# Optimization experiments

Measured on AMD Instinct MI355X. Metric: run time of the kernel, lower is better.

Reference implementation:

```python
import jax, jax.numpy as jnp
import numpy as np

OMEGA_ENC = 0.01   # Encoder.omega
OMEGA_K = 0.1      # KernelMLP.omega
N0, E0 = 4096, 16384     # level-0 graph
N1, E1 = 1024, 8192      # level-1 (pooled) graph
F_IN, H, LAT, DIM = 8, 64, 32, 3
F = H + DIM              # conv input features (x || pos)


def _glorot(key, shape):
    s = jnp.sqrt(2.0 / (shape[0] + shape[-1]))
    return (jax.random.normal(key, shape) * s).astype(jnp.float32)


def setup_inputs() -> dict:
    key = jax.random.key(0)
    ks = jax.random.split(key, 24)
    inp = {
        "x": jax.random.normal(ks[0], (N0, F_IN), jnp.float32),
        "pos": jax.random.normal(ks[1], (N0, DIM), jnp.float32),
        "edge_index": jax.random.randint(ks[2], (2, E0), 0, N0),
        "pool_edge_index1": jax.random.randint(ks[3], (2, E1), 0, N1),
        "pool_pos1": jax.random.normal(ks[4], (N1, DIM), jnp.float32),
        "pool_keep_idx0": jnp.sort(jax.random.randint(ks[5], (N1,), 0, N0)),
        "lin0_w": _glorot(ks[6], (F_IN, H)),
        "lin0_b": 0.01 * jax.random.normal(ks[7], (H,), jnp.float32),
        "lin1_w": _glorot(ks[8], (H, LAT)),
        "lin1_b": 0.01 * jax.random.normal(ks[9], (LAT,), jnp.float32),
    }
    k = 10
    for i in range(2):
        inp[f"conv{i}_k_w0"] = _glorot(ks[k], (DIM + 1, H))
        inp[f"conv{i}_k_b0"] = 0.01 * jax.random.normal(ks[k + 1], (H,), jnp.float32)
        inp[f"conv{i}_k_w1"] = _glorot(ks[k + 2], (H, H))
        inp[f"conv{i}_k_b1"] = 0.01 * jax.random.normal(ks[k + 3], (H,), jnp.float32)
        inp[f"conv{i}_k_w2"] = _glorot(ks[k + 4], (H, F))
        inp[f"conv{i}_k_b2"] = 0.01 * jax.random.normal(ks[k + 5], (F,), jnp.float32)
        inp[f"conv{i}_bias"] = jnp.zeros((H,), jnp.float32)  # zeros() init in torch
        k += 6
    return inp


def _with_self_loops(ei, n):
    # add_remaining_self_loops: input edges are assumed self-loop-free
    loops = jnp.arange(n, dtype=ei.dtype)
    return jnp.concatenate([ei, jnp.stack([loops, loops])], axis=1)


def _kernel_conv(xf, ei, pos, n, w0, b0, w1, b1, w2, b2, bias):
    src, dst = ei[0], ei[1]
    rel = pos[dst] - pos[src]                               # [E,3]
    zero = jnp.all(rel == 0.0, axis=1)                      # self loops -> rho=0, nan phi in torch
    rel_s = jnp.where(zero[:, None], 1.0, rel)              # safe values (avoid nan grads)
    rho = jnp.sqrt(jnp.sum(rel_s * rel_s, axis=1))
    theta = jnp.arctan2(rel_s[:, 1], rel_s[:, 0])
    phi = jnp.arcsin(jnp.clip(rel_s[:, 2] / rho, -1.0, 1.0))
    # torch sets theta/phi to 0 where phi is nan (rho==0); rho itself is 0 there
    rho = jnp.where(zero, 0.0, rho)
    theta = jnp.where(zero, 0.0, theta)
    phi = jnp.where(zero, 0.0, phi)
    feats = jnp.stack([rho, theta / jnp.pi, phi / jnp.pi], axis=1)   # [E,3]
    # KernelMLP lin0 on (feats || channel_id), evaluated for all out channels at once
    base = feats @ w0[:DIM] + b0                            # [E,H]
    ch = jnp.arange(H, dtype=xf.dtype)                      # out_channels == H
    h0 = jnp.sin(OMEGA_K * (base[None] + ch[:, None, None] * w0[DIM][None, None]))  # [C,E,H]
    h1 = jnp.sin(OMEGA_K * (jnp.einsum('ceh,hk->cek', h0, w1) + b1))                # [C,E,H]
    x_j = xf[src]                                           # [E,F]
    # msg[e,c] = (lin2(h1[c,e]) * x_j[e]).sum(); lin2 folded into the contraction
    msg = jnp.einsum('ceh,hf,ef->ec', h1, w2, x_j) + (x_j @ b2)[:, None]            # [E,C]
    return jax.ops.segment_sum(msg, dst, num_segments=n) + bias


def reference(x, edge_index, pos, pool_edge_index1, pool_pos1, pool_keep_idx0,
              lin0_w, lin0_b, lin1_w, lin1_b,
              conv0_k_w0, conv0_k_b0, conv0_k_w1, conv0_k_b1, conv0_k_w2, conv0_k_b2, conv0_bias,
              conv1_k_w0, conv1_k_b0, conv1_k_w1, conv1_k_b1, conv1_k_w2, conv1_k_b2, conv1_bias):
    n0 = x.shape[0]
    h = jnp.sin(OMEGA_ENC * (x @ lin0_w + lin0_b))
    ei0 = _with_self_loops(edge_index, n0)
    h = jnp.sin(OMEGA_ENC * _kernel_conv(jnp.concatenate([h, pos], 1), ei0, pos, n0,
                                         conv0_k_w0, conv0_k_b0, conv0_k_w1, conv0_k_b1,
                                         conv0_k_w2, conv0_k_b2, conv0_bias))
    # max_pool_neighbor_x: per-node max over neighbors incl. self (self loops in ei0)
    h = jax.ops.segment_max(h[ei0[0]], ei0[1], num_segments=n0)[pool_keep_idx0]
    n1 = pool_pos1.shape[0]
    ei1 = _with_self_loops(pool_edge_index1, n1)
    h = jnp.sin(OMEGA_ENC * _kernel_conv(jnp.concatenate([h, pool_pos1], 1), ei1, pool_pos1, n1,
                                         conv1_k_w0, conv1_k_b0, conv1_k_w1, conv1_k_b1,
                                         conv1_k_w2, conv1_k_b2, conv1_bias))
    return jnp.sin(OMEGA_ENC * (h @ lin1_w + lin1_b))   # [N1, LAT]
```

## Files before the change

kernel.cpp:

```cpp
#include <hip/hip_runtime.h>
#include <hip/hip_fp16.h>

#define N0C 4096
#define E0C 16384
#define N1C 1024
#define E1C 8192
#define HC 64
#define FINC 8
#define LATC 32
#define FC 67
#define E0T (E0C + N0C)
#define E1T (E1C + N1C)

typedef float f32x4 __attribute__((ext_vector_type(4)));
typedef _Float16 f16x8 __attribute__((ext_vector_type(8)));

__global__ __launch_bounds__(256) void k_prep(
    const float* __restrict__ x, const float* __restrict__ l0w,
    const float* __restrict__ l0b, const float* __restrict__ posp,
    const float* __restrict__ c0w2, const float* __restrict__ c0b2,
    const float* __restrict__ c0w0, const float* __restrict__ c1w0,
    const float* __restrict__ c0w1, const float* __restrict__ c1w1,
    const int* __restrict__ ei0, const int* __restrict__ ei1,
    _Float16* __restrict__ bC0, _Float16* __restrict__ bS0,
    _Float16* __restrict__ bC1, _Float16* __restrict__ bS1,
    _Float16* __restrict__ w1f0, _Float16* __restrict__ w1f1,
    int* __restrict__ cnt, float* __restrict__ tN, float* __restrict__ dN) {
  if (blockIdx.x < 1024) {
    __shared__ float w2s[64][69];
    __shared__ float xr[4][64];
    const int tid = threadIdx.x;
    const int wave = __builtin_amdgcn_readfirstlane(tid >> 6), lane = tid & 63;
    for (int idx = tid; idx < HC * FC; idx += 256)
      w2s[idx / FC][idx % FC] = c0w2[idx];
    const int n = blockIdx.x * 4 + wave;
    float a = l0b[lane];
#pragma unroll
    for (int f = 0; f < FINC; ++f) a = fmaf(x[n * FINC + f], l0w[f * HC + lane], a);
    xr[wave][lane] = sinf(0.01f * a);
    __syncthreads();
    const float px = posp[n * 3], py = posp[n * 3 + 1], pz = posp[n * 3 + 2];
    float tl = 0.f, ds = 0.f;
#pragma unroll 8
    for (int f = 0; f < HC; ++f) {
      float xv = xr[wave][f];
      tl = fmaf(xv, w2s[lane][f], tl);
      ds = fmaf(xv, c0b2[f], ds);
    }
    tl = fmaf(px, w2s[lane][64], fmaf(py, w2s[lane][65], fmaf(pz, w2s[lane][66], tl)));
    ds = fmaf(px, c0b2[64], fmaf(py, c0b2[65], fmaf(pz, c0b2[66], ds)));
    tN[n * HC + lane] = tl;
    if (lane == 0) dN[n] = ds;
  } else {
    int id = (blockIdx.x - 1024) * 256 + threadIdx.x;
    if (id < 8192) {
      int lvl = id >> 12, r = id & 4095;
      int fi = r >> 9, lane = (r >> 3) & 63, j = r & 7;
      int nt = fi & 3, ks = fi >> 2;
      int c = nt * 16 + (lane & 15);
      int h = ks * 32 + (lane >> 4) * 8 + j;
      const float* w = lvl ? c1w0 : c0w0;
      float s, cv;
      sincosf(0.1f * (float)c * w[3 * HC + h], &s, &cv);
      (lvl ? bC1 : bC0)[r] = (_Float16)cv;
      (lvl ? bS1 : bS0)[r] = (_Float16)s;
    } else if (id < 16384) {
      int r0 = id - 8192;
      int lvl = r0 >> 12, r = r0 & 4095;
      int fi = r >> 9, lane = (r >> 3) & 63, j = r & 7;
      int ms = fi & 3, ks = fi >> 2;
      int h = ks * 32 + (lane >> 4) * 8 + j;
      int kout = ms * 16 + (lane & 15);
      const float* w = lvl ? c1w1 : c0w1;
      (lvl ? w1f1 : w1f0)[r] = (_Float16)(0.1f * w[h * HC + kout]);
    } else if (id < 16384 + E0T + E1T) {
      int r = id - 16384;
      if (r < E0T) {
        int dst = (r < E0C) ? ei0[E0C + r] : (r - E0C);
        atomicAdd(cnt + dst, 1);
      } else {
        int e = r - E0T;
        int dst = (e < E1C) ? ei1[E1C + e] : (e - E1C);
        atomicAdd(cnt + N0C + dst, 1);
      }
    }
  }
}

__global__ void k_scan(const int* __restrict__ cnt, int* __restrict__ rp0,
                       int* __restrict__ rp1) {
  __shared__ int wsum[16];
  const int b = blockIdx.x;
  const int n = b ? N1C : N0C;
  const int* c = cnt + (b ? N0C : 0);
  int* rp = b ? rp1 : rp0;
  const int tid = threadIdx.x;
  const int lane = tid & 63, wid = tid >> 6;
  const int per = n >> 10;
  int loc[4];
  int sum = 0;
  for (int j = 0; j < per; ++j) { loc[j] = c[tid * per + j]; sum += loc[j]; }
  int xv = sum;
#pragma unroll
  for (int off = 1; off < 64; off <<= 1) {
    int v = __shfl_up(xv, off, 64);
    if (lane >= off) xv += v;
  }
  if (lane == 63) wsum[wid] = xv;
  __syncthreads();
  if (wid == 0) {
    int w = (lane < 16) ? wsum[lane] : 0;
#pragma unroll
    for (int off = 1; off < 16; off <<= 1) {
      int v = __shfl_up(w, off, 64);
      if (lane >= off) w += v;
    }
    if (lane < 16) wsum[lane] = w;
  }
  __syncthreads();
  int prefix = wid ? wsum[wid - 1] : 0;
  int incl = xv + prefix;
  int base = incl - sum;
  for (int j = 0; j < per; ++j) { rp[tid * per + j] = base; base += loc[j]; }
  if (tid == 1023) rp[n] = incl;
}

__global__ void k_scatter(const int* __restrict__ ei0, const int* __restrict__ ei1,
                          const int* __restrict__ rp0, const int* __restrict__ rp1,
                          int* __restrict__ fill, int* __restrict__ eidx0,
                          int* __restrict__ eidx1) {
  int id = blockIdx.x * blockDim.x + threadIdx.x;
  if (id < E0T) {
    int dst = (id < E0C) ? ei0[E0C + id] : (id - E0C);
    eidx0[rp0[dst] + atomicAdd(fill + dst, 1)] = id;
  } else if (id < E0T + E1T) {
    int e = id - E0T;
    int dst = (e < E1C) ? ei1[E1C + e] : (e - E1C);
    eidx1[rp1[dst] + atomicAdd(fill + N0C + dst, 1)] = e;
  }
}

__global__ __launch_bounds__(256, 3) void k_conv(
    const int* __restrict__ ei, int E,
    const float* __restrict__ posp,
    const float* __restrict__ tN, const float* __restrict__ dN,
    const float* __restrict__ kw0, const float* __restrict__ kb0,
    const _Float16* __restrict__ bC, const _Float16* __restrict__ bS,
    const _Float16* __restrict__ w1f, const float* __restrict__ b1,
    float* __restrict__ msg) {
  __shared__ __attribute__((aligned(16))) _Float16 bCs[4096], bSs[4096];
  __shared__ __attribute__((aligned(16))) _Float16 scS[4][2][64], scC[4][2][64];
  const int tid = threadIdx.x;
  const int wave = __builtin_amdgcn_readfirstlane(tid >> 6), lane = tid & 63;
  const int q = lane >> 4;
  for (int idx = tid; idx < 512; idx += 256) {
    ((f16x8*)bCs)[idx] = ((const f16x8*)bC)[idx];
    ((f16x8*)bSs)[idx] = ((const f16x8*)bS)[idx];
  }
  f16x8 w1r[8];
#pragma unroll
  for (int f = 0; f < 8; ++f) w1r[f] = *(const f16x8*)(w1f + ((f << 6) + lane) * 8);
  f32x4 bbq[4];
#pragma unroll
  for (int ms = 0; ms < 4; ++ms) {
    f32x4 t = *(const f32x4*)(b1 + ms * 16 + q * 4);
    bbq[ms] = t * 0.1f;
  }
  const float kb0v = kb0[lane];
  const float kw0x = kw0[lane], kw0y = kw0[HC + lane], kw0z = kw0[2 * HC + lane];
  __syncthreads();

  const int e0 = (blockIdx.x * 4 + wave) * 4;

  auto stg = [&](int e, int& sN, float& sv, float& cv, float& dv) {
    int s, d2;
    if (e < E) { s = ei[e]; d2 = ei[E + e]; } else { s = e - E; d2 = s; }
    sN = s;
    const float px = posp[s * 3], py = posp[s * 3 + 1], pz = posp[s * 3 + 2];
    const float rx = posp[d2 * 3] - px;
    const float ry = posp[d2 * 3 + 1] - py;
    const float rz = posp[d2 * 3 + 2] - pz;
    float f0 = 0.f, f1 = 0.f, f2 = 0.f;
    if (!(rx == 0.f && ry == 0.f && rz == 0.f)) {
      const float PI_F = 3.14159265358979323846f;
      float rho = sqrtf(rx * rx + ry * ry + rz * rz);
      float th = atan2f(ry, rx);
      float ratio = fminf(1.f, fmaxf(-1.f, rz / rho));
      float ph = asinf(ratio);
      f0 = rho; f1 = th / PI_F; f2 = ph / PI_F;
    }
    float base = fmaf(f0, kw0x, fmaf(f1, kw0y, fmaf(f2, kw0z, kb0v)));
    sincosf(0.1f * base, &sv, &cv);
    dv = dN[s];
  };

  int s0;
  float sv0, cv0, dv0;
  stg(e0, s0, sv0, cv0, dv0);
#pragma unroll
  for (int i = 0; i < 4; ++i) {
    const int buf = i & 1;
    scS[wave][buf][lane] = (_Float16)sv0;
    scC[wave][buf][lane] = (_Float16)cv0;
    __builtin_amdgcn_wave_barrier();
    f32x4 tr[4];
    {
      const float* trp = tN + (size_t)s0 * HC;
#pragma unroll
      for (int ms = 0; ms < 4; ++ms) tr[ms] = *(const f32x4*)(trp + ms * 16 + q * 4);
    }
    int s1 = 0;
    float sv1 = 0.f, cv1 = 0.f, dv1 = 0.f;
    if (i < 3) stg(e0 + i + 1, s1, sv1, cv1, dv1);

    f32x4 acc[4][4];
#pragma unroll
    for (int ms = 0; ms < 4; ++ms)
#pragma unroll
      for (int nt = 0; nt < 4; ++nt) acc[ms][nt] = bbq[ms];
#pragma unroll
    for (int ks = 0; ks < 2; ++ks) {
      f16x8 sv8 = *(const f16x8*)&scS[wave][buf][ks * 32 + q * 8];
      f16x8 cv8 = *(const f16x8*)&scC[wave][buf][ks * 32 + q * 8];
      f16x8 bf[4];
#pragma unroll
      for (int nt = 0; nt < 4; ++nt) {
        f16x8 cb = *(const f16x8*)&bCs[((ks * 4 + nt) * 64 + lane) * 8];
        f16x8 sb = *(const f16x8*)&bSs[((ks * 4 + nt) * 64 + lane) * 8];
        bf[nt] = sv8 * cb + cv8 * sb;
      }
#pragma unroll
      for (int ms = 0; ms < 4; ++ms)
#pragma unroll
        for (int nt = 0; nt < 4; ++nt)
          acc[ms][nt] = __builtin_amdgcn_mfma_f32_16x16x32_f16(
              w1r[ks * 4 + ms], bf[nt], acc[ms][nt], 0, 0, 0);
    }

    float snt0 = 0.f, snt1 = 0.f, snt2 = 0.f, snt3 = 0.f;
#pragma unroll
    for (int ms = 0; ms < 4; ++ms) {
#pragma unroll
      for (int r = 0; r < 4; ++r) {
        float tt = tr[ms][r];
        snt0 = fmaf(__sinf(acc[ms][0][r]), tt, snt0);
        snt1 = fmaf(__sinf(acc[ms][1][r]), tt, snt1);
        snt2 = fmaf(__sinf(acc[ms][2][r]), tt, snt2);
        snt3 = fmaf(__sinf(acc[ms][3][r]), tt, snt3);
      }
    }
    snt0 += __shfl_xor(snt0, 16, 64); snt0 += __shfl_xor(snt0, 32, 64);
    snt1 += __shfl_xor(snt1, 16, 64); snt1 += __shfl_xor(snt1, 32, 64);
    snt2 += __shfl_xor(snt2, 16, 64); snt2 += __shfl_xor(snt2, 32, 64);
    snt3 += __shfl_xor(snt3, 16, 64); snt3 += __shfl_xor(snt3, 32, 64);
    float val = (q == 0) ? snt0 : (q == 1) ? snt1 : (q == 2) ? snt2 : snt3;
    msg[(size_t)(e0 + i) * HC + lane] = val + dv0;
    s0 = s1; sv0 = sv1; cv0 = cv1; dv0 = dv1;
  }
}

__global__ void k_reduce0(const float* __restrict__ msg, const int* __restrict__ eidx,
                          const int* __restrict__ rp, const float* __restrict__ bias,
                          float* __restrict__ hc) {
  const int wave = threadIdx.x >> 6, lane = threadIdx.x & 63;
  const int n = blockIdx.x * 4 + wave;
  const int j0 = rp[n], j1 = rp[n + 1];
  float a0 = 0.f, a1 = 0.f;
  int j = j0;
  for (; j + 1 < j1; j += 2) {
    int ea = eidx[j], eb = eidx[j + 1];
    a0 += msg[(size_t)ea * HC + lane];
    a1 += msg[(size_t)eb * HC + lane];
  }
  if (j < j1) a0 += msg[(size_t)eidx[j] * HC + lane];
  hc[(size_t)n * HC + lane] = sinf(0.01f * (a0 + a1 + bias[lane]));
}

__global__ void k_pool1(const float* __restrict__ hc0, const int* __restrict__ eidx,
                        const int* __restrict__ rp, const int* __restrict__ ei,
                        const int* __restrict__ keep, const float* __restrict__ ppos,
                        const float* __restrict__ c1w2, const float* __restrict__ c1b2,
                        float* __restrict__ tN, float* __restrict__ dN) {
  __shared__ float w2s[64][69];
  __shared__ float xr[4][64];
  const int tid = threadIdx.x;
  const int wave = __builtin_amdgcn_readfirstlane(tid >> 6), lane = tid & 63;
  for (int idx = tid; idx < HC * FC; idx += 256)
    w2s[idx / FC][idx % FC] = c1w2[idx];
  const int i = blockIdx.x * 4 + wave;
  int n = keep[i];
  int j0 = rp[n], j1 = rp[n + 1];
  float m = -INFINITY;
  for (int j = j0; j < j1; ++j) {
    int e = eidx[j];
    int src = (e < E0C) ? ei[e] : (e - E0C);
    m = fmaxf(m, hc0[(size_t)src * HC + lane]);
  }
  xr[wave][lane] = m;
  __syncthreads();
  const float px = ppos[i * 3], py = ppos[i * 3 + 1], pz = ppos[i * 3 + 2];
  float tl = 0.f, ds = 0.f;
#pragma unroll 8
  for (int f = 0; f < HC; ++f) {
    float xv = xr[wave][f];
    tl = fmaf(xv, w2s[lane][f], tl);
    ds = fmaf(xv, c1b2[f], ds);
  }
  tl = fmaf(px, w2s[lane][64], fmaf(py, w2s[lane][65], fmaf(pz, w2s[lane][66], tl)));
  ds = fmaf(px, c1b2[64], fmaf(py, c1b2[65], fmaf(pz, c1b2[66], ds)));
  tN[i * HC + lane] = tl;
  if (lane == 0) dN[i] = ds;
}

__global__ void k_reduce1f(const float* __restrict__ msg, const int* __restrict__ eidx,
                           const int* __restrict__ rp, const float* __restrict__ bias,
                           const float* __restrict__ l1w, const float* __restrict__ l1b,
                           float* __restrict__ outp) {
  __shared__ float hr[4][64];
  const int wave = threadIdx.x >> 6, lane = threadIdx.x & 63;
  const int node = blockIdx.x * 4 + wave;
  const int j0 = rp[node], j1 = rp[node + 1];
  float a0 = 0.f, a1 = 0.f;
  int j = j0;
  for (; j + 1 < j1; j += 2) {
    int ea = eidx[j], eb = eidx[j + 1];
    a0 += msg[(size_t)ea * HC + lane];
    a1 += msg[(size_t)eb * HC + lane];
  }
  if (j < j1) a0 += msg[(size_t)eidx[j] * HC + lane];
  hr[wave][lane] = sinf(0.01f * (a0 + a1 + bias[lane]));
  __syncthreads();
  if (lane < LATC) {
    const float* h = hr[wave];
    float o = l1b[lane];
#pragma unroll 8
    for (int c = 0; c < HC; ++c) o = fmaf(h[c], l1w[c * LATC + lane], o);
    outp[node * LATC + lane] = sinf(0.01f * o);
  }
}

extern "C" void kernel_launch(void* const* d_in, const int* in_sizes, int n_in,
                              void* d_out, int out_size, void* d_ws, size_t ws_size,
                              hipStream_t stream) {
  (void)in_sizes; (void)n_in; (void)out_size; (void)ws_size;
  const float* x    = (const float*)d_in[0];
  const float* pos  = (const float*)d_in[1];
  const int*   ei   = (const int*)d_in[2];
  const int*   pei  = (const int*)d_in[3];
  const float* ppos = (const float*)d_in[4];
  const int*   keep = (const int*)d_in[5];
  const float* l0w  = (const float*)d_in[6];
  const float* l0b  = (const float*)d_in[7];
  const float* l1w  = (const float*)d_in[8];
  const float* l1b  = (const float*)d_in[9];
  const float* c0w0 = (const float*)d_in[10];
  const float* c0b0 = (const float*)d_in[11];
  const float* c0w1 = (const float*)d_in[12];
  const float* c0b1 = (const float*)d_in[13];
  const float* c0w2 = (const float*)d_in[14];
  const float* c0b2 = (const float*)d_in[15];
  const float* c0bias = (const float*)d_in[16];
  const float* c1w0 = (const float*)d_in[17];
  const float* c1b0 = (const float*)d_in[18];
  const float* c1w1 = (const float*)d_in[19];
  const float* c1b1 = (const float*)d_in[20];
  const float* c1w2 = (const float*)d_in[21];
  const float* c1b2 = (const float*)d_in[22];
  const float* c1bias = (const float*)d_in[23];
  float* outp = (float*)d_out;

  char* p = (char*)d_ws;
  auto carve = [&](size_t bytes) -> char* {
    char* r = p;
    p += (bytes + 255) & ~(size_t)255;
    return r;
  };
  float* hc0  = (float*)carve((size_t)N0C * HC * 4);
  float* tN0  = (float*)carve((size_t)N0C * HC * 4);
  float* dN0  = (float*)carve((size_t)N0C * 4);
  float* tN1  = (float*)carve((size_t)N1C * HC * 4);
  float* dN1  = (float*)carve((size_t)N1C * 4);
  _Float16* bC0  = (_Float16*)carve(4096 * 2);
  _Float16* bS0  = (_Float16*)carve(4096 * 2);
  _Float16* bC1  = (_Float16*)carve(4096 * 2);
  _Float16* bS1  = (_Float16*)carve(4096 * 2);
  _Float16* w1f0 = (_Float16*)carve(4096 * 2);
  _Float16* w1f1 = (_Float16*)carve(4096 * 2);
  int* cnt  = (int*)carve((size_t)(N0C + N1C) * 4);
  int* fill = (int*)carve((size_t)(N0C + N1C) * 4);
  int* rp0 = (int*)carve((size_t)(N0C + 1) * 4);
  int* rp1 = (int*)carve((size_t)(N1C + 1) * 4);
  int* eidx0 = (int*)carve((size_t)E0T * 4);
  int* eidx1 = (int*)carve((size_t)E1T * 4);
  float* msg = (float*)carve((size_t)E0T * HC * 4);

  hipMemsetAsync(cnt, 0, (size_t)(N0C + N1C) * 4 * 2, stream);

  k_prep<<<1024 + 180, 256, 0, stream>>>(x, l0w, l0b, pos, c0w2, c0b2,
                                         c0w0, c1w0, c0w1, c1w1, ei, pei,
                                         bC0, bS0, bC1, bS1, w1f0, w1f1,
                                         cnt, tN0, dN0);
  k_scan<<<2, 1024, 0, stream>>>(cnt, rp0, rp1);
  k_scatter<<<(E0T + E1T + 255) / 256, 256, 0, stream>>>(ei, pei, rp0, rp1, fill,
                                                         eidx0, eidx1);
  k_conv<<<E0T / 16, 256, 0, stream>>>(ei, E0C, pos, tN0, dN0, c0w0, c0b0,
                                       bC0, bS0, w1f0, c0b1, msg);
  k_reduce0<<<N0C / 4, 256, 0, stream>>>(msg, eidx0, rp0, c0bias, hc0);
  k_pool1<<<N1C / 4, 256, 0, stream>>>(hc0, eidx0, rp0, ei, keep, ppos,
                                       c1w2, c1b2, tN1, dN1);
  k_conv<<<E1T / 16, 256, 0, stream>>>(pei, E1C, ppos, tN1, dN1, c1w0, c1b0,
                                       bC1, bS1, w1f1, c1b1, msg);
  k_reduce1f<<<N1C / 4, 256, 0, stream>>>(msg, eidx1, rp1, c1bias, l1w, l1b, outp);
}
```

Baseline: 193.6 us.

## Write conv messages in CSR order and use grid-stride persistent conv waves

The scatter kernel now records each edge's CSR slot, and the conv kernel writes each message directly to that slot. The reducers can then read messages contiguously per node without the eidx indirection. The conv kernel becomes a grid-stride persistent loop with fixed grids (1024 and 512 blocks) and launch bounds raised to 4, which spreads the shared-memory table load over more edges. The prep kernel processes four nodes per wave so the w2 staging cost is amortised. In exchange it adds an extra inverse-index array, an extra load per edge, and scattered message writes.

```diff
diff --git a/kernel.cpp b/kernel.cpp
--- a/kernel.cpp
+++ b/kernel.cpp
@@ -26,33 +26,38 @@
     _Float16* __restrict__ bC1, _Float16* __restrict__ bS1,
     _Float16* __restrict__ w1f0, _Float16* __restrict__ w1f1,
     int* __restrict__ cnt, float* __restrict__ tN, float* __restrict__ dN) {
-  if (blockIdx.x < 1024) {
+  if (blockIdx.x < 256) {
     __shared__ float w2s[64][69];
     __shared__ float xr[4][64];
     const int tid = threadIdx.x;
     const int wave = __builtin_amdgcn_readfirstlane(tid >> 6), lane = tid & 63;
     for (int idx = tid; idx < HC * FC; idx += 256)
       w2s[idx / FC][idx % FC] = c0w2[idx];
-    const int n = blockIdx.x * 4 + wave;
-    float a = l0b[lane];
-#pragma unroll
-    for (int f = 0; f < FINC; ++f) a = fmaf(x[n * FINC + f], l0w[f * HC + lane], a);
-    xr[wave][lane] = sinf(0.01f * a);
     __syncthreads();
-    const float px = posp[n * 3], py = posp[n * 3 + 1], pz = posp[n * 3 + 2];
-    float tl = 0.f, ds = 0.f;
+#pragma unroll
+    for (int i = 0; i < 4; ++i) {
+      const int n = (blockIdx.x * 4 + wave) + i * 1024;
+      float a = l0b[lane];
+#pragma unroll
+      for (int f = 0; f < FINC; ++f) a = fmaf(x[n * FINC + f], l0w[f * HC + lane], a);
+      xr[wave][lane] = sinf(0.01f * a);
+      __builtin_amdgcn_wave_barrier();
+      const float px = posp[n * 3], py = posp[n * 3 + 1], pz = posp[n * 3 + 2];
+      float tl = 0.f, ds = 0.f;
 #pragma unroll 8
-    for (int f = 0; f < HC; ++f) {
-      float xv = xr[wave][f];
-      tl = fmaf(xv, w2s[lane][f], tl);
-      ds = fmaf(xv, c0b2[f], ds);
-    }
-    tl = fmaf(px, w2s[lane][64], fmaf(py, w2s[lane][65], fmaf(pz, w2s[lane][66], tl)));
-    ds = fmaf(px, c0b2[64], fmaf(py, c0b2[65], fmaf(pz, c0b2[66], ds)));
-    tN[n * HC + lane] = tl;
-    if (lane == 0) dN[n] = ds;
+      for (int f = 0; f < HC; ++f) {
+        float xv = xr[wave][f];
+        tl = fmaf(xv, w2s[lane][f], tl);
+        ds = fmaf(xv, c0b2[f], ds);
+      }
+      tl = fmaf(px, w2s[lane][64], fmaf(py, w2s[lane][65], fmaf(pz, w2s[lane][66], tl)));
+      ds = fmaf(px, c0b2[64], fmaf(py, c0b2[65], fmaf(pz, c0b2[66], ds)));
+      tN[n * HC + lane] = tl;
+      if (lane == 0) dN[n] = ds;
+      __builtin_amdgcn_wave_barrier();
+    }
   } else {
-    int id = (blockIdx.x - 1024) * 256 + threadIdx.x;
+    int id = (blockIdx.x - 256) * 256 + threadIdx.x;
     if (id < 8192) {
       int lvl = id >> 12, r = id & 4095;
       int fi = r >> 9, lane = (r >> 3) & 63, j = r & 7;
@@ -128,26 +133,31 @@
 __global__ void k_scatter(const int* __restrict__ ei0, const int* __restrict__ ei1,
                           const int* __restrict__ rp0, const int* __restrict__ rp1,
                           int* __restrict__ fill, int* __restrict__ eidx0,
-                          int* __restrict__ eidx1) {
+                          int* __restrict__ eidx1, int* __restrict__ inv0,
+                          int* __restrict__ inv1) {
   int id = blockIdx.x * blockDim.x + threadIdx.x;
   if (id < E0T) {
     int dst = (id < E0C) ? ei0[E0C + id] : (id - E0C);
-    eidx0[rp0[dst] + atomicAdd(fill + dst, 1)] = id;
+    int p = rp0[dst] + atomicAdd(fill + dst, 1);
+    eidx0[p] = id;
+    inv0[id] = p;
   } else if (id < E0T + E1T) {
     int e = id - E0T;
     int dst = (e < E1C) ? ei1[E1C + e] : (e - E1C);
-    eidx1[rp1[dst] + atomicAdd(fill + N0C + dst, 1)] = e;
-  }
-}
-
-__global__ __launch_bounds__(256, 3) void k_conv(
-    const int* __restrict__ ei, int E,
+    int p = rp1[dst] + atomicAdd(fill + N0C + dst, 1);
+    eidx1[p] = e;
+    inv1[e] = p;
+  }
+}
+
+__global__ __launch_bounds__(256, 4) void k_conv(
+    const int* __restrict__ ei, int E, int eTot,
     const float* __restrict__ posp,
     const float* __restrict__ tN, const float* __restrict__ dN,
     const float* __restrict__ kw0, const float* __restrict__ kb0,
     const _Float16* __restrict__ bC, const _Float16* __restrict__ bS,
     const _Float16* __restrict__ w1f, const float* __restrict__ b1,
-    float* __restrict__ msg) {
+    const int* __restrict__ inv, float* __restrict__ msg) {
   __shared__ __attribute__((aligned(16))) _Float16 bCs[4096], bSs[4096];
   __shared__ __attribute__((aligned(16))) _Float16 scS[4][2][64], scC[4][2][64];
   const int tid = threadIdx.x;
@@ -170,11 +180,13 @@
   const float kw0x = kw0[lane], kw0y = kw0[HC + lane], kw0z = kw0[2 * HC + lane];
   __syncthreads();
 
-  const int e0 = (blockIdx.x * 4 + wave) * 4;
-
-  auto stg = [&](int e, int& sN, float& sv, float& cv, float& dv) {
+  const int nW = gridDim.x * 4;
+  int e = blockIdx.x * 4 + wave;
+  if (e >= eTot) return;
+
+  auto stg = [&](int ee, int& sN, float& sv, float& cv, float& dv) {
     int s, d2;
-    if (e < E) { s = ei[e]; d2 = ei[E + e]; } else { s = e - E; d2 = s; }
+    if (ee < E) { s = ei[ee]; d2 = ei[E + ee]; } else { s = ee - E; d2 = s; }
     sN = s;
     const float px = posp[s * 3], py = posp[s * 3 + 1], pz = posp[s * 3 + 2];
     const float rx = posp[d2 * 3] - px;
@@ -196,22 +208,30 @@
 
   int s0;
   float sv0, cv0, dv0;
-  stg(e0, s0, sv0, cv0, dv0);
-#pragma unroll
-  for (int i = 0; i < 4; ++i) {
-    const int buf = i & 1;
-    scS[wave][buf][lane] = (_Float16)sv0;
-    scC[wave][buf][lane] = (_Float16)cv0;
-    __builtin_amdgcn_wave_barrier();
+  stg(e, s0, sv0, cv0, dv0);
+  int buf = 0;
+  scS[wave][0][lane] = (_Float16)sv0;
+  scC[wave][0][lane] = (_Float16)cv0;
+  __builtin_amdgcn_wave_barrier();
+
+  while (true) {
+    const int en = e + nW;
+    const bool more = en < eTot;
     f32x4 tr[4];
     {
       const float* trp = tN + (size_t)s0 * HC;
 #pragma unroll
       for (int ms = 0; ms < 4; ++ms) tr[ms] = *(const f32x4*)(trp + ms * 16 + q * 4);
     }
+    const int ip = inv[e];
     int s1 = 0;
     float sv1 = 0.f, cv1 = 0.f, dv1 = 0.f;
-    if (i < 3) stg(e0 + i + 1, s1, sv1, cv1, dv1);
+    if (more) {
+      stg(en, s1, sv1, cv1, dv1);
+      scS[wave][buf ^ 1][lane] = (_Float16)sv1;
+      scC[wave][buf ^ 1][lane] = (_Float16)cv1;
+    }
+    __builtin_amdgcn_wave_barrier();
 
     f32x4 acc[4][4];
 #pragma unroll
@@ -254,25 +274,27 @@
     snt2 += __shfl_xor(snt2, 16, 64); snt2 += __shfl_xor(snt2, 32, 64);
     snt3 += __shfl_xor(snt3, 16, 64); snt3 += __shfl_xor(snt3, 32, 64);
     float val = (q == 0) ? snt0 : (q == 1) ? snt1 : (q == 2) ? snt2 : snt3;
-    msg[(size_t)(e0 + i) * HC + lane] = val + dv0;
-    s0 = s1; sv0 = sv1; cv0 = cv1; dv0 = dv1;
-  }
-}
-
-__global__ void k_reduce0(const float* __restrict__ msg, const int* __restrict__ eidx,
-                          const int* __restrict__ rp, const float* __restrict__ bias,
-                          float* __restrict__ hc) {
+    msg[(size_t)ip * HC + lane] = val + dv0;
+
+    if (!more) break;
+    e = en; s0 = s1; dv0 = dv1; buf ^= 1;
+  }
+}
+
+__global__ void k_reduce0(const float* __restrict__ msg, const int* __restrict__ rp,
+                          const float* __restrict__ bias, float* __restrict__ hc) {
   const int wave = threadIdx.x >> 6, lane = threadIdx.x & 63;
   const int n = blockIdx.x * 4 + wave;
   const int j0 = rp[n], j1 = rp[n + 1];
+  const float* p = msg + (size_t)j0 * HC + lane;
+  const int m = j1 - j0;
   float a0 = 0.f, a1 = 0.f;
-  int j = j0;
-  for (; j + 1 < j1; j += 2) {
-    int ea = eidx[j], eb = eidx[j + 1];
-    a0 += msg[(size_t)ea * HC + lane];
-    a1 += msg[(size_t)eb * HC + lane];
-  }
-  if (j < j1) a0 += msg[(size_t)eidx[j] * HC + lane];
+  int j = 0;
+  for (; j + 1 < m; j += 2) {
+    a0 += p[(size_t)j * HC];
+    a1 += p[(size_t)(j + 1) * HC];
+  }
+  if (j < m) a0 += p[(size_t)j * HC];
   hc[(size_t)n * HC + lane] = sinf(0.01f * (a0 + a1 + bias[lane]));
 }
 
@@ -312,22 +334,22 @@
   if (lane == 0) dN[i] = ds;
 }
 
-__global__ void k_reduce1f(const float* __restrict__ msg, const int* __restrict__ eidx,
-                           const int* __restrict__ rp, const float* __restrict__ bias,
-                           const float* __restrict__ l1w, const float* __restrict__ l1b,
-                           float* __restrict__ outp) {
+__global__ void k_reduce1f(const float* __restrict__ msg, const int* __restrict__ rp,
+                           const float* __restrict__ bias, const float* __restrict__ l1w,
+                           const float* __restrict__ l1b, float* __restrict__ outp) {
   __shared__ float hr[4][64];
   const int wave = threadIdx.x >> 6, lane = threadIdx.x & 63;
   const int node = blockIdx.x * 4 + wave;
   const int j0 = rp[node], j1 = rp[node + 1];
+  const float* p = msg + (size_t)j0 * HC + lane;
+  const int m = j1 - j0;
   float a0 = 0.f, a1 = 0.f;
-  int j = j0;
-  for (; j + 1 < j1; j += 2) {
-    int ea = eidx[j], eb = eidx[j + 1];
-    a0 += msg[(size_t)ea * HC + lane];
-    a1 += msg[(size_t)eb * HC + lane];
-  }
-  if (j < j1) a0 += msg[(size_t)eidx[j] * HC + lane];
+  int j = 0;
+  for (; j + 1 < m; j += 2) {
+    a0 += p[(size_t)j * HC];
+    a1 += p[(size_t)(j + 1) * HC];
+  }
+  if (j < m) a0 += p[(size_t)j * HC];
   hr[wave][lane] = sinf(0.01f * (a0 + a1 + bias[lane]));
   __syncthreads();
   if (lane < LATC) {
@@ -392,23 +414,25 @@
   int* rp1 = (int*)carve((size_t)(N1C + 1) * 4);
   int* eidx0 = (int*)carve((size_t)E0T * 4);
   int* eidx1 = (int*)carve((size_t)E1T * 4);
+  int* inv0  = (int*)carve((size_t)E0T * 4);
+  int* inv1  = (int*)carve((size_t)E1T * 4);
   float* msg = (float*)carve((size_t)E0T * HC * 4);
 
   hipMemsetAsync(cnt, 0, (size_t)(N0C + N1C) * 4 * 2, stream);
 
-  k_prep<<<1024 + 180, 256, 0, stream>>>(x, l0w, l0b, pos, c0w2, c0b2,
-                                         c0w0, c1w0, c0w1, c1w1, ei, pei,
-                                         bC0, bS0, bC1, bS1, w1f0, w1f1,
-                                         cnt, tN0, dN0);
+  k_prep<<<256 + 180, 256, 0, stream>>>(x, l0w, l0b, pos, c0w2, c0b2,
+                                        c0w0, c1w0, c0w1, c1w1, ei, pei,
+                                        bC0, bS0, bC1, bS1, w1f0, w1f1,
+                                        cnt, tN0, dN0);
   k_scan<<<2, 1024, 0, stream>>>(cnt, rp0, rp1);
   k_scatter<<<(E0T + E1T + 255) / 256, 256, 0, stream>>>(ei, pei, rp0, rp1, fill,
-                                                         eidx0, eidx1);
-  k_conv<<<E0T / 16, 256, 0, stream>>>(ei, E0C, pos, tN0, dN0, c0w0, c0b0,
-                                       bC0, bS0, w1f0, c0b1, msg);
-  k_reduce0<<<N0C / 4, 256, 0, stream>>>(msg, eidx0, rp0, c0bias, hc0);
+                                                         eidx0, eidx1, inv0, inv1);
+  k_conv<<<1024, 256, 0, stream>>>(ei, E0C, E0T, pos, tN0, dN0, c0w0, c0b0,
+                                   bC0, bS0, w1f0, c0b1, inv0, msg);
+  k_reduce0<<<N0C / 4, 256, 0, stream>>>(msg, rp0, c0bias, hc0);
   k_pool1<<<N1C / 4, 256, 0, stream>>>(hc0, eidx0, rp0, ei, keep, ppos,
                                        c1w2, c1b2, tN1, dN1);
-  k_conv<<<E1T / 16, 256, 0, stream>>>(pei, E1C, ppos, tN1, dN1, c1w0, c1b0,
-                                       bC1, bS1, w1f1, c1b1, msg);
-  k_reduce1f<<<N1C / 4, 256, 0, stream>>>(msg, eidx1, rp1, c1bias, l1w, l1b, outp);
-}
+  k_conv<<<512, 256, 0, stream>>>(pei, E1C, E1T, ppos, tN1, dN1, c1w0, c1b0,
+                                  bC1, bS1, w1f1, c1b1, inv1, msg);
+  k_reduce1f<<<N1C / 4, 256, 0, stream>>>(msg, rp1, c1bias, l1w, l1b, outp);
+}
```

Result: slower. 285.1 us (+47.3%).
